# Optimization experiments

Hardware: AMD Instinct MI355X
Metric: run time of the kernel (lower is better)

Reference implementation:

```python
import jax, jax.numpy as jnp
import numpy as np


def setup_inputs() -> dict:
    key = jax.random.key(0)
    ks = jax.random.split(key, 6)
    B, N, D, E = 16, 64, 256, 256
    nodes = jax.random.normal(ks[0], (B * N, D), jnp.float32)
    edges = jax.random.normal(ks[1], (B * N * N, E), jnp.float32)
    W_in = jax.random.normal(ks[2], (2 * D + E, D), jnp.float32) / np.float32(np.sqrt(2 * D + E))
    b_in = jnp.zeros((D,), jnp.float32)
    W_coef = jax.random.normal(ks[3], (D, 1), jnp.float32) / np.float32(np.sqrt(D))
    b_coef = jnp.zeros((1,), jnp.float32)
    W_out = jax.random.normal(ks[4], (D, D), jnp.float32) / np.float32(np.sqrt(D))
    b_out = jnp.zeros((D,), jnp.float32)
    return {"nodes": nodes, "edges": edges, "W_in": W_in, "b_in": b_in,
            "W_coef": W_coef, "b_coef": b_coef, "W_out": W_out, "b_out": b_out,
            "B": B, "N": N}


def reference(nodes, edges, W_in, b_in, W_coef, b_coef, W_out, b_out, B, N):
    # Uniform nums = [N]*B special case of the ragged torch loop.
    D = nodes.shape[-1]
    n3 = nodes.reshape(B, N, D)
    # pair[b,i,j] = [node_i, node_j, edge_ij]  -> [B,N,N,2D+E]
    pair = jnp.concatenate([
        jnp.broadcast_to(n3[:, :, None, :], (B, N, N, D)),
        jnp.broadcast_to(n3[:, None, :, :], (B, N, N, D)),
        edges.reshape(B, N, N, -1),
    ], axis=-1)
    h = jax.nn.relu(pair @ W_in + b_in)            # [B,N,N,D]
    coefs = h @ W_coef + b_coef                    # [B,N,N,1]
    diag = jnp.eye(N, dtype=coefs.dtype)[None, :, :, None] * jnp.float32(1e9)
    attn = jax.nn.softmax(coefs - diag, axis=2)    # softmax over j, diag masked
    residual = jnp.sum(attn * h, axis=2)           # [B,N,D]
    new_nodes = nodes + jax.nn.relu(residual.reshape(B * N, D) @ W_out + b_out)
    return new_nodes, h.reshape(B * N * N, D)
```

## Files before the change

### kernel.cpp

```cpp
#include <hip/hip_runtime.h>
#include <hip/hip_bf16.h>

typedef unsigned int u32;
typedef unsigned short u16;
typedef __attribute__((ext_vector_type(8))) short bf16x8;
typedef __attribute__((ext_vector_type(4))) float f32x4;
typedef __attribute__((ext_vector_type(4))) float f4;

#define DI __device__ __forceinline__

DI u16 f2bfu(float f){
  union{float f; u32 i;} u; u.f = f;
  u32 lsb = (u.i >> 16) & 1u;
  u.i += 0x7fffu + lsb;
  return (u16)(u.i >> 16);
}

union BU { uint4 v; bf16x8 s; };

DI void gld16(const void* g, void* l){
  __builtin_amdgcn_global_load_lds(
      (const __attribute__((address_space(1))) void*)g,
      (__attribute__((address_space(3))) void*)l, 16, 0, 0);
}

__global__ __launch_bounds__(256) void k_pack(const float* __restrict__ W_in,
                                              u16* __restrict__ Wp3,
                                              u16* __restrict__ Wp12)
{
  int idx = blockIdx.x * 256 + threadIdx.x;
  int l = idx & 63;
  int g = idx >> 6;
  int lq = l >> 4, lr = l & 15;
  u16 o[8];
  if (g < 128){
    int nt = g >> 3, kk = g & 7;
    int n  = nt * 16 + lr;
    int k0 = 512 + kk * 32 + lq * 8;
#pragma unroll
    for (int tt = 0; tt < 8; tt++) o[tt] = f2bfu(W_in[(size_t)(k0 + tt) * 256 + n]);
    *(uint4*)(Wp3 + (size_t)idx * 8) = *(uint4*)o;
  } else {
    int g2 = g - 128;
    int half = g2 >> 7, rem = g2 & 127;
    int nt = rem >> 3, kk = rem & 7;
    int n  = nt * 16 + lr;
    int k0 = half * 256 + kk * 32 + lq * 8;
#pragma unroll
    for (int tt = 0; tt < 8; tt++) o[tt] = f2bfu(W_in[(size_t)(k0 + tt) * 256 + n]);
    *(uint4*)(Wp12 + (size_t)g2 * 512 + (size_t)l * 8) = *(uint4*)o;
  }
}

__global__ __launch_bounds__(256) void k_pre(
    const float* __restrict__ nodes, const float* __restrict__ b_in,
    const u16* __restrict__ Wp12, float* __restrict__ P1, float* __restrict__ P2)
{
  const int t = threadIdx.x;
  const int w = t >> 6, l = t & 63, lq = l >> 4, lr = l & 15;
  const int bid = blockIdx.x;
  const int rt = bid >> 3, half = (bid >> 2) & 1, cg = bid & 3;

  bf16x8 af[8];
  {
    const float* ap = nodes + (size_t)(rt * 64 + 16 * w + lr) * 256 + lq * 8;
#pragma unroll
    for (int kk = 0; kk < 8; kk++){
      float4 x = *(const float4*)(ap + kk * 32);
      float4 y = *(const float4*)(ap + kk * 32 + 4);
      bf16x8 a;
      a[0]=(short)f2bfu(x.x); a[1]=(short)f2bfu(x.y); a[2]=(short)f2bfu(x.z); a[3]=(short)f2bfu(x.w);
      a[4]=(short)f2bfu(y.x); a[5]=(short)f2bfu(y.y); a[6]=(short)f2bfu(y.z); a[7]=(short)f2bfu(y.w);
      af[kk] = a;
    }
  }
  const uint4* wp = (const uint4*)(Wp12 + (size_t)half * 128 * 512);
  float* P = half ? P2 : P1;
#pragma unroll
  for (int ntl = 0; ntl < 4; ntl++){
    const int nt = cg * 4 + ntl;
    f32x4 acc = {0.f, 0.f, 0.f, 0.f};
#pragma unroll
    for (int kk = 0; kk < 8; kk++){
      BU bu; bu.v = wp[(nt * 8 + kk) * 64 + l];
      acc = __builtin_amdgcn_mfma_f32_16x16x32_bf16(af[kk], bu.s, acc, 0, 0, 0);
    }
    const int col = nt * 16 + lr;
    const float bv = half ? 0.f : b_in[col];
#pragma unroll
    for (int r = 0; r < 4; r++){
      const int row = rt * 64 + 16 * w + 4 * lq + r;
      P[(size_t)row * 256 + col] = acc[r] + bv;
    }
  }
}

__global__ __launch_bounds__(256, 3) void k_h(
    const float* __restrict__ edges, const u16* __restrict__ Wp3,
    const float* __restrict__ W_coef, const float* __restrict__ P1,
    const float* __restrict__ P2, float* __restrict__ out_h,
    float* __restrict__ coefW)
{
  __shared__ uint4 wS[2][1024];

  const int t = threadIdx.x;
  const int w = t >> 6, l = t & 63, lq = l >> 4, lr = l & 15;
  const int bid = blockIdx.x;
  const int bi = ((bid & 7) << 7) | (bid >> 3);
  const int b = bi >> 6;
  const int j = 16 * w + lr;

  const char* wp3b = (const char*)Wp3;
  auto stage = [&](int bufi, int ntc){
    const char* src = wp3b + (size_t)ntc * 16384;
    char* dst = (char*)&wS[bufi][0];
#pragma unroll
    for (int c = 0; c < 4; ++c)
      gld16(src + (w * 4 + c) * 1024 + l * 16, dst + (w * 4 + c) * 1024);
  };

  stage(0, 0);

  bf16x8 af[8];
  {
    const float* ap = edges + (size_t)bi * 16384 + (size_t)j * 256 + lq * 8;
    float4 x[4], y[4];
#pragma unroll
    for (int kk = 0; kk < 4; kk++){
      x[kk] = *(const float4*)(ap + kk * 32);
      y[kk] = *(const float4*)(ap + kk * 32 + 4);
    }
#pragma unroll
    for (int kk = 0; kk < 4; kk++){
      bf16x8 a;
      a[0]=(short)f2bfu(x[kk].x); a[1]=(short)f2bfu(x[kk].y); a[2]=(short)f2bfu(x[kk].z); a[3]=(short)f2bfu(x[kk].w);
      a[4]=(short)f2bfu(y[kk].x); a[5]=(short)f2bfu(y[kk].y); a[6]=(short)f2bfu(y[kk].z); a[7]=(short)f2bfu(y[kk].w);
      af[kk] = a;
    }
#pragma unroll
    for (int kk = 0; kk < 4; kk++){
      x[kk] = *(const float4*)(ap + (kk + 4) * 32);
      y[kk] = *(const float4*)(ap + (kk + 4) * 32 + 4);
    }
#pragma unroll
    for (int kk = 0; kk < 4; kk++){
      bf16x8 a;
      a[0]=(short)f2bfu(x[kk].x); a[1]=(short)f2bfu(x[kk].y); a[2]=(short)f2bfu(x[kk].z); a[3]=(short)f2bfu(x[kk].w);
      a[4]=(short)f2bfu(y[kk].x); a[5]=(short)f2bfu(y[kk].y); a[6]=(short)f2bfu(y[kk].z); a[7]=(short)f2bfu(y[kk].w);
      af[kk + 4] = a;
    }
  }

  const float* p1p = P1 + (size_t)bi * 256;
  const float* p2p = P2 + ((size_t)b * 64 + j) * 256;
  float* hop = out_h + ((size_t)bi * 64 + j) * 256;
  float cpart = 0.f;

  __syncthreads();
  int buf = 0;
#pragma unroll
  for (int ntc = 0; ntc < 8; ntc++){
    if (ntc < 7) stage(buf ^ 1, ntc + 1);
#pragma unroll
    for (int nt2 = 0; nt2 < 2; nt2++){
      const int nt = ntc * 2 + nt2;
      f32x4 acc = {0.f, 0.f, 0.f, 0.f};
#pragma unroll
      for (int kk = 0; kk < 8; kk++){
        BU bu; bu.v = wS[buf][(nt2 * 8 + kk) * 64 + l];
        acc = __builtin_amdgcn_mfma_f32_16x16x32_bf16(bu.s, af[kk], acc, 0, 0, 0);
      }
      const int d0 = nt * 16 + 4 * lq;
      f4 p1v = *(const f4*)(p1p + d0);
      f4 p2v = *(const f4*)(p2p + d0);
      f4 wcv = *(const f4*)(W_coef + d0);
      f4 h;
#pragma unroll
      for (int r = 0; r < 4; r++){
        float xx = acc[r] + p1v[r] + p2v[r];
        h[r] = xx > 0.f ? xx : 0.f;
      }
      *(f4*)(hop + d0) = h;
      cpart += h[0]*wcv[0] + h[1]*wcv[1] + h[2]*wcv[2] + h[3]*wcv[3];
    }
    __syncthreads();
    buf ^= 1;
  }

  cpart += __shfl_xor(cpart, 16, 64);
  cpart += __shfl_xor(cpart, 32, 64);
  if (lq == 0) coefW[(size_t)bi * 64 + j] = cpart;
}

__global__ __launch_bounds__(256) void k_attn(
    const float* __restrict__ nodes, const float* __restrict__ coefW,
    const float* __restrict__ b_coef, const float* __restrict__ W_out,
    const float* __restrict__ b_out, const float* __restrict__ h_in,
    float* __restrict__ out_nodes)
{
  __shared__ float attnS[64];
  __shared__ float resS[256];

  const int t = threadIdx.x;
  const int bid = blockIdx.x;
  const int bi = ((bid & 7) << 7) | (127 - (bid >> 3));
  const int i = bi & 63;

  if (t < 64){
    float val = coefW[(size_t)bi * 64 + t] + b_coef[0] - (t == i ? 1e9f : 0.f);
    float m = val;
#pragma unroll
    for (int off = 32; off >= 1; off >>= 1){ float o = __shfl_xor(m, off, 64); m = m > o ? m : o; }
    float e = __expf(val - m);
    float s = e;
#pragma unroll
    for (int off = 32; off >= 1; off >>= 1) s += __shfl_xor(s, off, 64);
    attnS[t] = e / s;
  }
  __syncthreads();

  {
    const float* hb = h_in + (size_t)bi * 16384;
    float res = 0.f;
#pragma unroll 8
    for (int jj = 0; jj < 64; jj++) res += attnS[jj] * hb[(size_t)jj * 256 + t];
    resS[t] = res;
  }
  __syncthreads();

  {
    const int d = t;
    float acco = b_out[d];
#pragma unroll 8
    for (int k4 = 0; k4 < 64; k4++){
      float4 r4 = *(const float4*)&resS[k4 * 4];
      acco += r4.x * W_out[(size_t)(k4 * 4 + 0) * 256 + d];
      acco += r4.y * W_out[(size_t)(k4 * 4 + 1) * 256 + d];
      acco += r4.z * W_out[(size_t)(k4 * 4 + 2) * 256 + d];
      acco += r4.w * W_out[(size_t)(k4 * 4 + 3) * 256 + d];
    }
    float nv = nodes[(size_t)bi * 256 + d];
    out_nodes[(size_t)bi * 256 + d] = nv + (acco > 0.f ? acco : 0.f);
  }
}

extern "C" void kernel_launch(void* const* d_in, const int* in_sizes, int n_in,
                              void* d_out, int out_size, void* d_ws, size_t ws_size,
                              hipStream_t stream)
{
  const float* nodes  = (const float*)d_in[0];
  const float* edges  = (const float*)d_in[1];
  const float* W_in   = (const float*)d_in[2];
  const float* b_in   = (const float*)d_in[3];
  const float* W_coef = (const float*)d_in[4];
  const float* b_coef = (const float*)d_in[5];
  const float* W_out  = (const float*)d_in[6];
  const float* b_out  = (const float*)d_in[7];
  (void)in_sizes; (void)n_in; (void)out_size; (void)ws_size;

  float* P1  = (float*)d_ws;
  float* P2  = P1 + 262144;
  u16*  Wp3  = (u16*)(P2 + 262144);
  u16*  Wp12 = Wp3 + 65536;
  float* coefW = (float*)(Wp12 + 131072);

  float* out_nodes = (float*)d_out;
  float* out_h = out_nodes + 262144;

  hipLaunchKernelGGL(k_pack, dim3(96),   dim3(256), 0, stream, W_in, Wp3, Wp12);
  hipLaunchKernelGGL(k_pre,  dim3(128),  dim3(256), 0, stream, nodes, b_in, Wp12, P1, P2);
  hipLaunchKernelGGL(k_h,    dim3(1024), dim3(256), 0, stream,
                     edges, Wp3, W_coef, P1, P2, out_h, coefW);
  hipLaunchKernelGGL(k_attn, dim3(1024), dim3(256), 0, stream,
                     nodes, coefW, b_coef, W_out, b_out, out_h, out_nodes);
}
```

Baseline: 178.2 us.

## Drop LDS weight staging in k_h, halve block size, split output projection kernel

k_h now uses 128-thread blocks (2048 of them) that read the packed bf16 weights straight from global/L2 instead of double-buffering them through LDS with barriers. The intent is to raise occupancy and remove synchronisation. The cost is more global and L2 weight traffic per block. The attention kernel now only writes the residual, and a new k_out kernel applies W_out to 4 rows per block so each W_out load is reused four times. This adds one kernel launch and a round trip through the workspace for RES.

Result: slower. 200.4 us (+12.5%).

```diff
diff --git a/kernel.cpp b/kernel.cpp
--- a/kernel.cpp
+++ b/kernel.cpp
@@ -17,12 +17,6 @@
 }
 
 union BU { uint4 v; bf16x8 s; };
-
-DI void gld16(const void* g, void* l){
-  __builtin_amdgcn_global_load_lds(
-      (const __attribute__((address_space(1))) void*)g,
-      (__attribute__((address_space(3))) void*)l, 16, 0, 0);
-}
 
 __global__ __launch_bounds__(256) void k_pack(const float* __restrict__ W_in,
                                               u16* __restrict__ Wp3,
@@ -95,31 +89,22 @@
   }
 }
 
-__global__ __launch_bounds__(256, 3) void k_h(
+__global__ __launch_bounds__(128, 6) void k_h(
     const float* __restrict__ edges, const u16* __restrict__ Wp3,
     const float* __restrict__ W_coef, const float* __restrict__ P1,
     const float* __restrict__ P2, float* __restrict__ out_h,
     float* __restrict__ coefW)
 {
-  __shared__ uint4 wS[2][1024];
-
   const int t = threadIdx.x;
   const int w = t >> 6, l = t & 63, lq = l >> 4, lr = l & 15;
   const int bid = blockIdx.x;
-  const int bi = ((bid & 7) << 7) | (bid >> 3);
+  const int xcd  = bid & 7;
+  const int rest = bid >> 3;
+  const int jh   = rest & 1;
+  const int bi   = (xcd << 7) | (rest >> 1);
   const int b = bi >> 6;
-  const int j = 16 * w + lr;
-
-  const char* wp3b = (const char*)Wp3;
-  auto stage = [&](int bufi, int ntc){
-    const char* src = wp3b + (size_t)ntc * 16384;
-    char* dst = (char*)&wS[bufi][0];
-#pragma unroll
-    for (int c = 0; c < 4; ++c)
-      gld16(src + (w * 4 + c) * 1024 + l * 16, dst + (w * 4 + c) * 1024);
-  };
-
-  stage(0, 0);
+  const int jq = jh * 2 + w;
+  const int j  = jq * 16 + lr;
 
   bf16x8 af[8];
   {
@@ -151,23 +136,21 @@
     }
   }
 
+  const uint4* wp = (const uint4*)Wp3;
   const float* p1p = P1 + (size_t)bi * 256;
   const float* p2p = P2 + ((size_t)b * 64 + j) * 256;
   float* hop = out_h + ((size_t)bi * 64 + j) * 256;
   float cpart = 0.f;
 
-  __syncthreads();
-  int buf = 0;
 #pragma unroll
   for (int ntc = 0; ntc < 8; ntc++){
-    if (ntc < 7) stage(buf ^ 1, ntc + 1);
 #pragma unroll
     for (int nt2 = 0; nt2 < 2; nt2++){
       const int nt = ntc * 2 + nt2;
       f32x4 acc = {0.f, 0.f, 0.f, 0.f};
 #pragma unroll
       for (int kk = 0; kk < 8; kk++){
-        BU bu; bu.v = wS[buf][(nt2 * 8 + kk) * 64 + l];
+        BU bu; bu.v = wp[(size_t)(nt * 8 + kk) * 64 + l];
         acc = __builtin_amdgcn_mfma_f32_16x16x32_bf16(bu.s, af[kk], acc, 0, 0, 0);
       }
       const int d0 = nt * 16 + 4 * lq;
@@ -183,8 +166,6 @@
       *(f4*)(hop + d0) = h;
       cpart += h[0]*wcv[0] + h[1]*wcv[1] + h[2]*wcv[2] + h[3]*wcv[3];
     }
-    __syncthreads();
-    buf ^= 1;
   }
 
   cpart += __shfl_xor(cpart, 16, 64);
@@ -193,13 +174,10 @@
 }
 
 __global__ __launch_bounds__(256) void k_attn(
-    const float* __restrict__ nodes, const float* __restrict__ coefW,
-    const float* __restrict__ b_coef, const float* __restrict__ W_out,
-    const float* __restrict__ b_out, const float* __restrict__ h_in,
-    float* __restrict__ out_nodes)
+    const float* __restrict__ coefW, const float* __restrict__ b_coef,
+    const float* __restrict__ h_in, float* __restrict__ RES)
 {
   __shared__ float attnS[64];
-  __shared__ float resS[256];
 
   const int t = threadIdx.x;
   const int bid = blockIdx.x;
@@ -222,26 +200,38 @@
   {
     const float* hb = h_in + (size_t)bi * 16384;
     float res = 0.f;
+#pragma unroll 16
+    for (int jj = 0; jj < 64; jj++) res += attnS[jj] * hb[(size_t)jj * 256 + t];
+    RES[(size_t)bi * 256 + t] = res;
+  }
+}
+
+__global__ __launch_bounds__(256) void k_out(
+    const float* __restrict__ nodes, const float* __restrict__ RES,
+    const float* __restrict__ W_out, const float* __restrict__ b_out,
+    float* __restrict__ out_nodes)
+{
+  __shared__ float sR[4][256];
+  const int t = threadIdx.x;
+  const int r0 = blockIdx.x * 4;
+#pragma unroll
+  for (int r = 0; r < 4; r++) sR[r][t] = RES[(size_t)(r0 + r) * 256 + t];
+  __syncthreads();
+
+  const float bv = b_out[t];
+  float a0 = bv, a1 = bv, a2 = bv, a3 = bv;
 #pragma unroll 8
-    for (int jj = 0; jj < 64; jj++) res += attnS[jj] * hb[(size_t)jj * 256 + t];
-    resS[t] = res;
-  }
-  __syncthreads();
-
-  {
-    const int d = t;
-    float acco = b_out[d];
-#pragma unroll 8
-    for (int k4 = 0; k4 < 64; k4++){
-      float4 r4 = *(const float4*)&resS[k4 * 4];
-      acco += r4.x * W_out[(size_t)(k4 * 4 + 0) * 256 + d];
-      acco += r4.y * W_out[(size_t)(k4 * 4 + 1) * 256 + d];
-      acco += r4.z * W_out[(size_t)(k4 * 4 + 2) * 256 + d];
-      acco += r4.w * W_out[(size_t)(k4 * 4 + 3) * 256 + d];
-    }
-    float nv = nodes[(size_t)bi * 256 + d];
-    out_nodes[(size_t)bi * 256 + d] = nv + (acco > 0.f ? acco : 0.f);
-  }
+  for (int k = 0; k < 256; k++){
+    const float wv = W_out[(size_t)k * 256 + t];
+    a0 += sR[0][k] * wv;
+    a1 += sR[1][k] * wv;
+    a2 += sR[2][k] * wv;
+    a3 += sR[3][k] * wv;
+  }
+  out_nodes[(size_t)(r0 + 0) * 256 + t] = nodes[(size_t)(r0 + 0) * 256 + t] + (a0 > 0.f ? a0 : 0.f);
+  out_nodes[(size_t)(r0 + 1) * 256 + t] = nodes[(size_t)(r0 + 1) * 256 + t] + (a1 > 0.f ? a1 : 0.f);
+  out_nodes[(size_t)(r0 + 2) * 256 + t] = nodes[(size_t)(r0 + 2) * 256 + t] + (a2 > 0.f ? a2 : 0.f);
+  out_nodes[(size_t)(r0 + 3) * 256 + t] = nodes[(size_t)(r0 + 3) * 256 + t] + (a3 > 0.f ? a3 : 0.f);
 }
 
 extern "C" void kernel_launch(void* const* d_in, const int* in_sizes, int n_in,
@@ -263,14 +253,17 @@
   u16*  Wp3  = (u16*)(P2 + 262144);
   u16*  Wp12 = Wp3 + 65536;
   float* coefW = (float*)(Wp12 + 131072);
+  float* RES   = coefW + 65536;
 
   float* out_nodes = (float*)d_out;
   float* out_h = out_nodes + 262144;
 
   hipLaunchKernelGGL(k_pack, dim3(96),   dim3(256), 0, stream, W_in, Wp3, Wp12);
   hipLaunchKernelGGL(k_pre,  dim3(128),  dim3(256), 0, stream, nodes, b_in, Wp12, P1, P2);
-  hipLaunchKernelGGL(k_h,    dim3(1024), dim3(256), 0, stream,
+  hipLaunchKernelGGL(k_h,    dim3(2048), dim3(128), 0, stream,
                      edges, Wp3, W_coef, P1, P2, out_h, coefW);
   hipLaunchKernelGGL(k_attn, dim3(1024), dim3(256), 0, stream,
-                     nodes, coefW, b_coef, W_out, b_out, out_h, out_nodes);
-}
+                     coefW, b_coef, out_h, RES);
+  hipLaunchKernelGGL(k_out,  dim3(256),  dim3(256), 0, stream,
+                     nodes, RES, W_out, b_out, out_nodes);
+}
```
